# Optimization experiments

Hardware: AMD Instinct MI355X
Metric: run time of the kernel (lower is better)

Reference implementation:

```python
import jax, jax.numpy as jnp
import numpy as np

VOCAB, EMB, HID = 32000, 128, 256
B, T = 512, 512


def setup_inputs() -> dict:
    key = jax.random.key(0)
    ks = jax.random.split(key, 6)
    x = jax.random.randint(ks[0], (B, T), 0, VOCAB, dtype=jnp.int64) if jax.config.jax_enable_x64 else jax.random.randint(ks[0], (B, T), 0, VOCAB, dtype=jnp.int32)
    s_e = 1.0 / np.sqrt(HID)
    emb = jax.random.normal(ks[1], (VOCAB, EMB), dtype=jnp.float32)
    W_ih = jax.random.uniform(ks[2], (3 * HID, EMB), dtype=jnp.float32, minval=-s_e, maxval=s_e)
    W_hh = jax.random.uniform(ks[3], (3 * HID, HID), dtype=jnp.float32, minval=-s_e, maxval=s_e)
    b_ih = jax.random.uniform(ks[4], (3 * HID,), dtype=jnp.float32, minval=-s_e, maxval=s_e)
    b_hh = jax.random.uniform(ks[5], (3 * HID,), dtype=jnp.float32, minval=-s_e, maxval=s_e)
    return {"x": x, "emb": emb, "W_ih": W_ih, "W_hh": W_hh, "b_ih": b_ih, "b_hh": b_hh}


def reference(x, emb, W_ih, W_hh, b_ih, b_hh):
    # in_len = x.shape[0] per original code (loops x[:, t, :] for t in range(x.shape[0]))
    in_len = x.shape[0]
    H = W_hh.shape[1]
    xe = emb[x]                                   # [B, T, E]
    xs = jnp.swapaxes(xe[:, :in_len, :], 0, 1)    # [in_len, B, E]
    # precompute input-side gate projections for all timesteps (one big GEMM)
    gi = jnp.einsum('tbe,ge->tbg', xs, W_ih) + b_ih   # [in_len, B, 3H]

    def step(h, gi_t):
        gh = h @ W_hh.T + b_hh                    # [B, 3H]
        i_r, i_z, i_n = gi_t[:, :H], gi_t[:, H:2*H], gi_t[:, 2*H:]
        h_r, h_z, h_n = gh[:, :H], gh[:, H:2*H], gh[:, 2*H:]
        r = jax.nn.sigmoid(i_r + h_r)
        z = jax.nn.sigmoid(i_z + h_z)
        n = jnp.tanh(i_n + r * h_n)
        h_new = (1.0 - z) * n + z * h
        return h_new, None

    h0 = jnp.zeros((x.shape[0], H), dtype=emb.dtype)  # batch = x.shape[0]
    hT, _ = jax.lax.scan(step, h0, gi)
    return hT
```

## Files before the change

### kernel.cpp

```cpp
#include <hip/hip_runtime.h>


typedef unsigned short ushort_t;
typedef __attribute__((ext_vector_type(8))) short short8;
typedef __attribute__((ext_vector_type(4))) float float4_;
typedef __attribute__((ext_vector_type(4))) unsigned short ushort4_;
typedef __attribute__((ext_vector_type(2))) unsigned int uint2_;

#define VOCAB 32000
#define EMB 128
#define HID 256
#define G3 768
#define BB 512
#define TT 512
#define SLOT 786432
#define BLK_BYTES 24576
#define WFIXED 8781824

__device__ __forceinline__ float b2f(ushort_t u) {
  return __uint_as_float(((unsigned)u) << 16);
}
__device__ __forceinline__ ushort_t f2b(float f) {
  unsigned u = __float_as_uint(f);
  return (ushort_t)((u + 0x7FFFu + ((u >> 16) & 1u)) >> 16);
}
__device__ __forceinline__ short8 ld8(const ushort_t* p) { return *(const short8*)p; }
__device__ __forceinline__ void gld_lds16(const void* g, void* l) {
  __builtin_amdgcn_global_load_lds((const __attribute__((address_space(1))) void*)g,
                                   (__attribute__((address_space(3))) void*)l, 16, 0, 0);
}
__device__ __forceinline__ int gi_byte(int bl, int twog) {
  return ((bl * 1536) + twog) ^ ((bl & 7) << 4);
}

__global__ void cvt_bf16_k(const float* __restrict__ s, ushort_t* __restrict__ d, int n4) {
  int i = blockIdx.x * blockDim.x + threadIdx.x;
  int stride = gridDim.x * blockDim.x;
  for (; i < n4; i += stride) {
    float4_ v = ((const float4_*)s)[i];
    ushort4_ o;
    o.x = f2b(v.x); o.y = f2b(v.y); o.z = f2b(v.z); o.w = f2b(v.w);
    ((ushort4_*)d)[i] = o;
  }
}

__global__ __launch_bounds__(256) void gi_gemm(
    const int* __restrict__ x, const ushort_t* __restrict__ emb16,
    const ushort_t* __restrict__ Wih16, const float* __restrict__ bih,
    const float* __restrict__ bhh, char* __restrict__ gic, int t0, int C) {
  __shared__ float cb[G3];
  __shared__ alignas(16) char img[2][BLK_BYTES];
  const int tid = threadIdx.x;
  for (int i = tid; i < G3; i += 256) cb[i] = bih[i] + (i < 512 ? bhh[i] : 0.f);
  const int lane = tid & 63, w = tid >> 6;
  const int bl = lane & 15, kg = lane >> 4;
  const int blk = blockIdx.x & 31;
  const int tt0 = (blockIdx.x >> 5) * 2;
  const int nj = (C - tt0) < 2 ? 1 : 2;

  short8 bfr[2][4];
#pragma unroll
  for (int j = 0; j < 2; ++j) {
    int tloc = tt0 + (j < nj ? j : 0);
    int tok = x[(blk * 16 + bl) * TT + t0 + tloc];
#pragma unroll
    for (int kt = 0; kt < 4; ++kt)
      bfr[j][kt] = ld8(emb16 + (size_t)tok * EMB + kt * 32 + kg * 8);
  }
  __syncthreads();

#pragma unroll 1
  for (int mi = 0; mi < 12; ++mi) {
    int mt = w * 12 + mi;
    short8 af[4];
#pragma unroll
    for (int kt = 0; kt < 4; ++kt)
      af[kt] = ld8(Wih16 + (mt * 16 + bl) * EMB + kt * 32 + kg * 8);
    float4_ z4 = {0.f, 0.f, 0.f, 0.f};
    float4_ acc[2] = {z4, z4};
#pragma unroll
    for (int kt = 0; kt < 4; ++kt)
#pragma unroll
      for (int j = 0; j < 2; ++j)
        acc[j] = __builtin_amdgcn_mfma_f32_16x16x32_bf16(af[kt], bfr[j][kt], acc[j], 0, 0, 0);
    int byte8 = gi_byte(bl, 32 * mt + 8 * kg);
#pragma unroll
    for (int j = 0; j < 2; ++j) {
      ushort4_ o;
#pragma unroll
      for (int r = 0; r < 4; ++r) o[r] = f2b(acc[j][r] + cb[mt * 16 + kg * 4 + r]);
      *(ushort4_*)(&img[j][byte8]) = o;
    }
  }
  __syncthreads();

#pragma unroll
  for (int j = 0; j < 2; ++j) {
    if (j < nj) {
      char* dst = gic + (size_t)(tt0 + j) * SLOT + (size_t)blk * BLK_BYTES;
#pragma unroll
      for (int c = 0; c < 6; ++c)
        *(float4_*)(dst + c * 4096 + tid * 16) = *(const float4_*)(&img[j][c * 4096 + tid * 16]);
    }
  }
}

__global__ __launch_bounds__(512, 2) void gru_rec(
    const ushort_t* __restrict__ Whh16, const char* __restrict__ gic,
    const float* __restrict__ bhh, float* __restrict__ out, int t0, int C) {
  __shared__ alignas(16) ushort_t h_lds[2][16 * HID];
  __shared__ alignas(16) char gi_ring[4][BLK_BYTES];

  const int tid = threadIdx.x, lane = tid & 63, w = tid >> 6;
  const int bl = lane & 15, kg = lane >> 4;
  const int b0 = blockIdx.x * 16;
  const char* gblk = gic + (size_t)blockIdx.x * BLK_BYTES;

  if (t0 == 0) {
    for (int i = tid; i < 16 * HID; i += 512) h_lds[0][i] = 0;
  } else {
    for (int i = tid; i < 16 * HID; i += 512) {
      int b = i >> 8, k = i & 255;
      *(ushort_t*)((char*)h_lds[0] + (((b << 9) + 2 * k) ^ ((b & 7) << 4))) =
          f2b(out[(size_t)(b0 + b) * HID + k]);
    }
  }

  short8 wf[2][3][8];
#pragma unroll
  for (int i = 0; i < 2; ++i)
#pragma unroll
    for (int q = 0; q < 3; ++q) {
      int g = (w + 8 * i + 16 * q) * 16 + bl;
#pragma unroll
      for (int kt = 0; kt < 8; ++kt)
        wf[i][q][kt] = ld8(Whh16 + (size_t)g * HID + kt * 32 + kg * 8);
    }

  float4_ bhn[2];
  float hreg[2][4];
#pragma unroll
  for (int i = 0; i < 2; ++i) {
    bhn[i] = *(const float4_*)&bhh[512 + (w + 8 * i) * 16 + kg * 4];
    if (t0 == 0) {
#pragma unroll
      for (int r = 0; r < 4; ++r) hreg[i][r] = 0.f;
    } else {
      float4_ v = *(const float4_*)&out[(size_t)(b0 + bl) * HID + (w + 8 * i) * 16 + kg * 4];
#pragma unroll
      for (int r = 0; r < 4; ++r) hreg[i][r] = v[r];
    }
  }

  asm volatile("s_waitcnt vmcnt(0) lgkmcnt(0)" ::: "memory");
  __builtin_amdgcn_s_barrier();
  __builtin_amdgcn_sched_barrier(0);

#pragma unroll
  for (int tau = 0; tau < 3; ++tau) {
    if (tau < C) {
      const char* src = gblk + (size_t)tau * SLOT + (w * 3) * 1024 + lane * 16;
      char* dst = &gi_ring[tau][(w * 3) * 1024];
#pragma unroll
      for (int ii = 0; ii < 3; ++ii) gld_lds16(src + ii * 1024, dst + ii * 1024);
    }
  }

#pragma unroll 1
  for (int t = 0; t < C; ++t) {
    int rem = C - 1 - t;
    if (rem >= 2)
      asm volatile("s_waitcnt vmcnt(6) lgkmcnt(0)" ::: "memory");
    else if (rem == 1)
      asm volatile("s_waitcnt vmcnt(3) lgkmcnt(0)" ::: "memory");
    else
      asm volatile("s_waitcnt vmcnt(0) lgkmcnt(0)" ::: "memory");
    __builtin_amdgcn_s_barrier();
    __builtin_amdgcn_sched_barrier(0);

    const int slot = t & 3, cur = t & 1, nxt = cur ^ 1;
    if (t + 3 < C) {
      const char* src = gblk + (size_t)(t + 3) * SLOT + (w * 3) * 1024 + lane * 16;
      char* dst = &gi_ring[(t + 3) & 3][(w * 3) * 1024];
#pragma unroll
      for (int ii = 0; ii < 3; ++ii) gld_lds16(src + ii * 1024, dst + ii * 1024);
    }

    float4_ acc[2][3];
#pragma unroll
    for (int i = 0; i < 2; ++i) {
#pragma unroll
      for (int q = 0; q < 2; ++q) {
        int byte8 = gi_byte(bl, 32 * (w + 8 * i + 16 * q) + 8 * kg);
        ushort4_ v = *(const ushort4_*)(&gi_ring[slot][byte8]);
#pragma unroll
        for (int r = 0; r < 4; ++r) acc[i][q][r] = b2f(v[r]);
      }
      acc[i][2] = bhn[i];
    }

#pragma unroll
    for (int kt = 0; kt < 8; ++kt) {
      int byteoff = ((bl * 512) + kt * 64 + kg * 16) ^ ((bl & 7) << 4);
      short8 bf = *(const short8*)((const char*)h_lds[cur] + byteoff);
#pragma unroll
      for (int i = 0; i < 2; ++i)
#pragma unroll
        for (int q = 0; q < 3; ++q)
          acc[i][q] = __builtin_amdgcn_mfma_f32_16x16x32_bf16(wf[i][q][kt], bf, acc[i][q], 0, 0, 0);
    }

#pragma unroll
    for (int i = 0; i < 2; ++i) {
      int byte8n = gi_byte(bl, 32 * (32 + w + 8 * i) + 8 * kg);
      ushort4_ gv = *(const ushort4_*)(&gi_ring[slot][byte8n]);
#pragma unroll
      for (int r = 0; r < 4; ++r) {
        float rr = __builtin_amdgcn_rcpf(1.f + __expf(-acc[i][0][r]));
        float zz = __builtin_amdgcn_rcpf(1.f + __expf(-acc[i][1][r]));
        float y = b2f(gv[r]) + rr * acc[i][2][r];
        float nn = 1.f - 2.f * __builtin_amdgcn_rcpf(1.f + __expf(2.f * y));
        hreg[i][r] = (1.f - zz) * nn + zz * hreg[i][r];
      }
      int byte0 = (bl * 512 + ((w + 8 * i) * 16 + kg * 4) * 2) ^ ((bl & 7) << 4);
      uint2_ hv;
      hv.x = (unsigned)f2b(hreg[i][0]) | ((unsigned)f2b(hreg[i][1]) << 16);
      hv.y = (unsigned)f2b(hreg[i][2]) | ((unsigned)f2b(hreg[i][3]) << 16);
      *(uint2_*)((char*)h_lds[nxt] + byte0) = hv;
    }
  }

#pragma unroll
  for (int i = 0; i < 2; ++i) {
    float4_ v = {hreg[i][0], hreg[i][1], hreg[i][2], hreg[i][3]};
    *(float4_*)&out[(size_t)(b0 + bl) * HID + (w + 8 * i) * 16 + kg * 4] = v;
  }
}

extern "C" void kernel_launch(void* const* d_in, const int* in_sizes, int n_in,
                              void* d_out, int out_size, void* d_ws, size_t ws_size,
                              hipStream_t stream) {
  const int* x = (const int*)d_in[0];
  const float* emb = (const float*)d_in[1];
  const float* Wih = (const float*)d_in[2];
  const float* Whh = (const float*)d_in[3];
  const float* bih = (const float*)d_in[4];
  const float* bhh = (const float*)d_in[5];
  float* out = (float*)d_out;

  char* ws = (char*)d_ws;
  ushort_t* emb16 = (ushort_t*)ws;
  ushort_t* Wih16 = (ushort_t*)(ws + 8192000);
  ushort_t* Whh16 = (ushort_t*)(ws + 8388608);
  char* gic = ws + WFIXED;

  size_t avail = ws_size > (size_t)WFIXED ? ws_size - (size_t)WFIXED : 0;
  int C = (int)(avail / (size_t)SLOT);
  if (C > TT) C = TT;
  if (C < 1) C = 1;

  cvt_bf16_k<<<1024, 256, 0, stream>>>(emb, emb16, (VOCAB * EMB) / 4);
  cvt_bf16_k<<<96, 256, 0, stream>>>(Wih, Wih16, (G3 * EMB) / 4);
  cvt_bf16_k<<<192, 256, 0, stream>>>(Whh, Whh16, (G3 * HID) / 4);

  for (int t0 = 0; t0 < TT; t0 += C) {
    int Cc = TT - t0 < C ? TT - t0 : C;
    gi_gemm<<<((Cc + 1) / 2) * 32, 256, 0, stream>>>(x, emb16, Wih16, bih, bhh, gic, t0, Cc);
    gru_rec<<<32, 512, 0, stream>>>(Whh16, gic, bhh, out, t0, Cc);
  }
}
```

Baseline: 1.521 ms.

## Precompute per-vocab input projection table and gather rows in recurrence

Replaces the per-(timestep,batch) input-gate GEMM with a table of W_ih·emb+bias over all 32000 vocab entries. The recurrent kernel then stages tokens in LDS and gathers table rows into its LDS ring with async global-to-LDS loads. This removes the large per-step gi buffer and the chunked launch loop, running the whole sequence in a single recurrence launch. In exchange the table GEMM does 32000 rows of work instead of 512x512, and each step's gathers hit scattered table rows rather than contiguous slots.

```diff
diff --git a/kernel.cpp b/kernel.cpp
--- a/kernel.cpp
+++ b/kernel.cpp
@@ -6,16 +6,15 @@
 typedef __attribute__((ext_vector_type(4))) float float4_;
 typedef __attribute__((ext_vector_type(4))) unsigned short ushort4_;
 typedef __attribute__((ext_vector_type(2))) unsigned int uint2_;
+typedef __attribute__((ext_vector_type(4))) int int4_;
 
 #define VOCAB 32000
 #define EMB 128
 #define HID 256
 #define G3 768
-#define BB 512
 #define TT 512
-#define SLOT 786432
-#define BLK_BYTES 24576
-#define WFIXED 8781824
+#define HB 98304
+#define XB 114688
 
 __device__ __forceinline__ float b2f(ushort_t u) {
   return __uint_as_float(((unsigned)u) << 16);
@@ -29,8 +28,8 @@
   __builtin_amdgcn_global_load_lds((const __attribute__((address_space(1))) void*)g,
                                    (__attribute__((address_space(3))) void*)l, 16, 0, 0);
 }
-__device__ __forceinline__ int gi_byte(int bl, int twog) {
-  return ((bl * 1536) + twog) ^ ((bl & 7) << 4);
+__device__ __forceinline__ int gi_byte(int bl, int c) {
+  return ((bl * 1536) + c) ^ ((bl & 7) << 4);
 }
 
 __global__ void cvt_bf16_k(const float* __restrict__ s, ushort_t* __restrict__ d, int n4) {
@@ -44,29 +43,22 @@
   }
 }
 
-__global__ __launch_bounds__(256) void gi_gemm(
-    const int* __restrict__ x, const ushort_t* __restrict__ emb16,
-    const ushort_t* __restrict__ Wih16, const float* __restrict__ bih,
-    const float* __restrict__ bhh, char* __restrict__ gic, int t0, int C) {
-  __shared__ float cb[G3];
-  __shared__ alignas(16) char img[2][BLK_BYTES];
+__global__ __launch_bounds__(256) void tbl_gemm(
+    const ushort_t* __restrict__ emb16, const ushort_t* __restrict__ Wih16,
+    const float* __restrict__ bih, const float* __restrict__ bhh,
+    char* __restrict__ tb_out) {
+  __shared__ float cbs[G3];
+  __shared__ alignas(16) char img[16 * 1552];
   const int tid = threadIdx.x;
-  for (int i = tid; i < G3; i += 256) cb[i] = bih[i] + (i < 512 ? bhh[i] : 0.f);
+  for (int i = tid; i < G3; i += 256) cbs[i] = bih[i] + (i < 512 ? bhh[i] : 0.f);
   const int lane = tid & 63, w = tid >> 6;
   const int bl = lane & 15, kg = lane >> 4;
-  const int blk = blockIdx.x & 31;
-  const int tt0 = (blockIdx.x >> 5) * 2;
-  const int nj = (C - tt0) < 2 ? 1 : 2;
-
-  short8 bfr[2][4];
-#pragma unroll
-  for (int j = 0; j < 2; ++j) {
-    int tloc = tt0 + (j < nj ? j : 0);
-    int tok = x[(blk * 16 + bl) * TT + t0 + tloc];
-#pragma unroll
-    for (int kt = 0; kt < 4; ++kt)
-      bfr[j][kt] = ld8(emb16 + (size_t)tok * EMB + kt * 32 + kg * 8);
-  }
+  const int v0 = blockIdx.x * 16;
+
+  short8 bfr[4];
+#pragma unroll
+  for (int kt = 0; kt < 4; ++kt)
+    bfr[kt] = ld8(emb16 + (size_t)(v0 + bl) * EMB + kt * 32 + kg * 8);
   __syncthreads();
 
 #pragma unroll 1
@@ -76,55 +68,48 @@
 #pragma unroll
     for (int kt = 0; kt < 4; ++kt)
       af[kt] = ld8(Wih16 + (mt * 16 + bl) * EMB + kt * 32 + kg * 8);
-    float4_ z4 = {0.f, 0.f, 0.f, 0.f};
-    float4_ acc[2] = {z4, z4};
+    float4_ acc = {0.f, 0.f, 0.f, 0.f};
 #pragma unroll
     for (int kt = 0; kt < 4; ++kt)
-#pragma unroll
-      for (int j = 0; j < 2; ++j)
-        acc[j] = __builtin_amdgcn_mfma_f32_16x16x32_bf16(af[kt], bfr[j][kt], acc[j], 0, 0, 0);
-    int byte8 = gi_byte(bl, 32 * mt + 8 * kg);
-#pragma unroll
-    for (int j = 0; j < 2; ++j) {
-      ushort4_ o;
-#pragma unroll
-      for (int r = 0; r < 4; ++r) o[r] = f2b(acc[j][r] + cb[mt * 16 + kg * 4 + r]);
-      *(ushort4_*)(&img[j][byte8]) = o;
-    }
+      acc = __builtin_amdgcn_mfma_f32_16x16x32_bf16(af[kt], bfr[kt], acc, 0, 0, 0);
+    int g0 = mt * 16 + kg * 4;
+    ushort4_ o;
+#pragma unroll
+    for (int r = 0; r < 4; ++r) o[r] = f2b(acc[r] + cbs[g0 + r]);
+    *(ushort4_*)(img + bl * 1552 + mt * 32 + kg * 8) = o;
   }
   __syncthreads();
 
 #pragma unroll
-  for (int j = 0; j < 2; ++j) {
-    if (j < nj) {
-      char* dst = gic + (size_t)(tt0 + j) * SLOT + (size_t)blk * BLK_BYTES;
-#pragma unroll
-      for (int c = 0; c < 6; ++c)
-        *(float4_*)(dst + c * 4096 + tid * 16) = *(const float4_*)(&img[j][c * 4096 + tid * 16]);
-    }
+  for (int c = 0; c < 6; ++c) {
+    int p = c * 4096 + tid * 16;
+    int q = p >> 9;
+    int row = (q * 21846) >> 16;
+    int off = p - row * 1536;
+    float4_ v = *(const float4_*)(img + row * 1552 + off);
+    *(float4_*)(tb_out + (size_t)(v0 + row) * 1536 + off) = v;
   }
 }
 
 __global__ __launch_bounds__(512, 2) void gru_rec(
-    const ushort_t* __restrict__ Whh16, const char* __restrict__ gic,
-    const float* __restrict__ bhh, float* __restrict__ out, int t0, int C) {
-  __shared__ alignas(16) ushort_t h_lds[2][16 * HID];
-  __shared__ alignas(16) char gi_ring[4][BLK_BYTES];
+    const ushort_t* __restrict__ Whh16, const char* __restrict__ tbl,
+    const float* __restrict__ bhh, const int* __restrict__ x,
+    float* __restrict__ out) {
+  __shared__ alignas(16) char smem[147456];
 
   const int tid = threadIdx.x, lane = tid & 63, w = tid >> 6;
   const int bl = lane & 15, kg = lane >> 4;
   const int b0 = blockIdx.x * 16;
-  const char* gblk = gic + (size_t)blockIdx.x * BLK_BYTES;
-
-  if (t0 == 0) {
-    for (int i = tid; i < 16 * HID; i += 512) h_lds[0][i] = 0;
-  } else {
-    for (int i = tid; i < 16 * HID; i += 512) {
-      int b = i >> 8, k = i & 255;
-      *(ushort_t*)((char*)h_lds[0] + (((b << 9) + 2 * k) ^ ((b & 7) << 4))) =
-          f2b(out[(size_t)(b0 + b) * HID + k]);
-    }
-  }
+
+  {
+    const int4_* xs = (const int4_*)(x + (size_t)b0 * TT);
+    int4_* xd = (int4_*)(smem + XB);
+#pragma unroll
+    for (int i = 0; i < 4; ++i) xd[tid + i * 512] = xs[tid + i * 512];
+    int4_ z4 = {0, 0, 0, 0};
+    *(int4_*)(smem + HB + tid * 16) = z4;
+  }
+  __syncthreads();
 
   short8 wf[2][3][8];
 #pragma unroll
@@ -142,33 +127,35 @@
 #pragma unroll
   for (int i = 0; i < 2; ++i) {
     bhn[i] = *(const float4_*)&bhh[512 + (w + 8 * i) * 16 + kg * 4];
-    if (t0 == 0) {
-#pragma unroll
-      for (int r = 0; r < 4; ++r) hreg[i][r] = 0.f;
-    } else {
-      float4_ v = *(const float4_*)&out[(size_t)(b0 + bl) * HID + (w + 8 * i) * 16 + kg * 4];
-#pragma unroll
-      for (int r = 0; r < 4; ++r) hreg[i][r] = v[r];
-    }
-  }
-
-  asm volatile("s_waitcnt vmcnt(0) lgkmcnt(0)" ::: "memory");
-  __builtin_amdgcn_s_barrier();
-  __builtin_amdgcn_sched_barrier(0);
+#pragma unroll
+    for (int r = 0; r < 4; ++r) hreg[i][r] = 0.f;
+  }
+
+  const int s0 = ((2 * w) & 7) << 4, s1 = ((2 * w + 1) & 7) << 4;
+  const unsigned inv0 = (unsigned)((lane * 16) ^ s0);
+  const unsigned inv1 = (lane < 32) ? (unsigned)((1024 + lane * 16) ^ s0)
+                                    : (unsigned)((lane * 16 - 512) ^ s1);
+  const unsigned inv2 = (unsigned)((512 + lane * 16) ^ s1);
+  const int* xtA = (const int*)(smem + XB) + (2 * w) * TT;
+  const int* xtB = (const int*)(smem + XB) + (2 * w + 1) * TT;
+
+  asm volatile("s_waitcnt vmcnt(0)" ::: "memory");
 
 #pragma unroll
   for (int tau = 0; tau < 3; ++tau) {
-    if (tau < C) {
-      const char* src = gblk + (size_t)tau * SLOT + (w * 3) * 1024 + lane * 16;
-      char* dst = &gi_ring[tau][(w * 3) * 1024];
-#pragma unroll
-      for (int ii = 0; ii < 3; ++ii) gld_lds16(src + ii * 1024, dst + ii * 1024);
-    }
+    int tokA = xtA[tau], tokB = xtB[tau];
+    const char* pA = tbl + (unsigned)tokA * 1536u;
+    const char* pB = tbl + (unsigned)tokB * 1536u;
+    const char* pM = (lane < 32) ? pA : pB;
+    char* d0 = smem + tau * 24576 + w * 3072;
+    gld_lds16(pA + inv0, d0);
+    gld_lds16(pM + inv1, d0 + 1024);
+    gld_lds16(pB + inv2, d0 + 2048);
   }
 
 #pragma unroll 1
-  for (int t = 0; t < C; ++t) {
-    int rem = C - 1 - t;
+  for (int t = 0; t < TT; ++t) {
+    int rem = TT - 1 - t;
     if (rem >= 2)
       asm volatile("s_waitcnt vmcnt(6) lgkmcnt(0)" ::: "memory");
     else if (rem == 1)
@@ -179,12 +166,18 @@
     __builtin_amdgcn_sched_barrier(0);
 
     const int slot = t & 3, cur = t & 1, nxt = cur ^ 1;
-    if (t + 3 < C) {
-      const char* src = gblk + (size_t)(t + 3) * SLOT + (w * 3) * 1024 + lane * 16;
-      char* dst = &gi_ring[(t + 3) & 3][(w * 3) * 1024];
-#pragma unroll
-      for (int ii = 0; ii < 3; ++ii) gld_lds16(src + ii * 1024, dst + ii * 1024);
-    }
+    if (t + 3 < TT) {
+      int tokA = xtA[t + 3], tokB = xtB[t + 3];
+      const char* pA = tbl + (unsigned)tokA * 1536u;
+      const char* pB = tbl + (unsigned)tokB * 1536u;
+      const char* pM = (lane < 32) ? pA : pB;
+      char* d0 = smem + ((t + 3) & 3) * 24576 + w * 3072;
+      gld_lds16(pA + inv0, d0);
+      gld_lds16(pM + inv1, d0 + 1024);
+      gld_lds16(pB + inv2, d0 + 2048);
+    }
+
+    const char* gtile = smem + slot * 24576;
 
     float4_ acc[2][3];
 #pragma unroll
@@ -192,7 +185,7 @@
 #pragma unroll
       for (int q = 0; q < 2; ++q) {
         int byte8 = gi_byte(bl, 32 * (w + 8 * i + 16 * q) + 8 * kg);
-        ushort4_ v = *(const ushort4_*)(&gi_ring[slot][byte8]);
+        ushort4_ v = *(const ushort4_*)(gtile + byte8);
 #pragma unroll
         for (int r = 0; r < 4; ++r) acc[i][q][r] = b2f(v[r]);
       }
@@ -202,7 +195,7 @@
 #pragma unroll
     for (int kt = 0; kt < 8; ++kt) {
       int byteoff = ((bl * 512) + kt * 64 + kg * 16) ^ ((bl & 7) << 4);
-      short8 bf = *(const short8*)((const char*)h_lds[cur] + byteoff);
+      short8 bf = *(const short8*)(smem + HB + cur * 8192 + byteoff);
 #pragma unroll
       for (int i = 0; i < 2; ++i)
 #pragma unroll
@@ -213,7 +206,7 @@
 #pragma unroll
     for (int i = 0; i < 2; ++i) {
       int byte8n = gi_byte(bl, 32 * (32 + w + 8 * i) + 8 * kg);
-      ushort4_ gv = *(const ushort4_*)(&gi_ring[slot][byte8n]);
+      ushort4_ gv = *(const ushort4_*)(gtile + byte8n);
 #pragma unroll
       for (int r = 0; r < 4; ++r) {
         float rr = __builtin_amdgcn_rcpf(1.f + __expf(-acc[i][0][r]));
@@ -226,7 +219,7 @@
       uint2_ hv;
       hv.x = (unsigned)f2b(hreg[i][0]) | ((unsigned)f2b(hreg[i][1]) << 16);
       hv.y = (unsigned)f2b(hreg[i][2]) | ((unsigned)f2b(hreg[i][3]) << 16);
-      *(uint2_*)((char*)h_lds[nxt] + byte0) = hv;
+      *(uint2_*)(smem + HB + nxt * 8192 + byte0) = hv;
     }
   }
 
@@ -252,20 +245,11 @@
   ushort_t* emb16 = (ushort_t*)ws;
   ushort_t* Wih16 = (ushort_t*)(ws + 8192000);
   ushort_t* Whh16 = (ushort_t*)(ws + 8388608);
-  char* gic = ws + WFIXED;
-
-  size_t avail = ws_size > (size_t)WFIXED ? ws_size - (size_t)WFIXED : 0;
-  int C = (int)(avail / (size_t)SLOT);
-  if (C > TT) C = TT;
-  if (C < 1) C = 1;
+  char* tbl = ws + 8781824;
 
   cvt_bf16_k<<<1024, 256, 0, stream>>>(emb, emb16, (VOCAB * EMB) / 4);
   cvt_bf16_k<<<96, 256, 0, stream>>>(Wih, Wih16, (G3 * EMB) / 4);
   cvt_bf16_k<<<192, 256, 0, stream>>>(Whh, Whh16, (G3 * HID) / 4);
-
-  for (int t0 = 0; t0 < TT; t0 += C) {
-    int Cc = TT - t0 < C ? TT - t0 : C;
-    gi_gemm<<<((Cc + 1) / 2) * 32, 256, 0, stream>>>(x, emb16, Wih16, bih, bhh, gic, t0, Cc);
-    gru_rec<<<32, 512, 0, stream>>>(Whh16, gic, bhh, out, t0, Cc);
-  }
-}
+  tbl_gemm<<<2000, 256, 0, stream>>>(emb16, Wih16, bih, bhh, tbl);
+  gru_rec<<<32, 512, 0, stream>>>(Whh16, tbl, bhh, x, out);
+}
```

Measured after the change: 1.361 ms. 1.12x faster.

## Precompute per-vocabulary input gate table and gather rows instead of per-token GEMM

Applied to the files above, without the earlier changes.

Computes the input-side gate projection (with biases) once for every vocabulary entry into a bf16 table, then builds the per-timestep gate buffer by gathering table rows by token id. This removes the redundant per-token GEMM, since there are far more tokens than vocabulary entries. In exchange it adds a ~49MB table write and random-row gather reads, and reduces the workspace left for timestep chunks, which may increase the number of chunks.

```diff
diff --git a/kernel.cpp b/kernel.cpp
--- a/kernel.cpp
+++ b/kernel.cpp
@@ -6,16 +6,17 @@
 typedef __attribute__((ext_vector_type(4))) float float4_;
 typedef __attribute__((ext_vector_type(4))) unsigned short ushort4_;
 typedef __attribute__((ext_vector_type(2))) unsigned int uint2_;
+typedef __attribute__((ext_vector_type(4))) int int4_;
 
 #define VOCAB 32000
 #define EMB 128
 #define HID 256
 #define G3 768
-#define BB 512
 #define TT 512
 #define SLOT 786432
 #define BLK_BYTES 24576
-#define WFIXED 8781824
+#define TBL_OFF 8781824
+#define GIC_OFF 57933824
 
 __device__ __forceinline__ float b2f(ushort_t u) {
   return __uint_as_float(((unsigned)u) << 16);
@@ -29,8 +30,8 @@
   __builtin_amdgcn_global_load_lds((const __attribute__((address_space(1))) void*)g,
                                    (__attribute__((address_space(3))) void*)l, 16, 0, 0);
 }
-__device__ __forceinline__ int gi_byte(int bl, int twog) {
-  return ((bl * 1536) + twog) ^ ((bl & 7) << 4);
+__device__ __forceinline__ int gi_byte(int bl, int c) {
+  return ((bl * 1536) + c) ^ ((bl & 7) << 4);
 }
 
 __global__ void cvt_bf16_k(const float* __restrict__ s, ushort_t* __restrict__ d, int n4) {
@@ -44,29 +45,22 @@
   }
 }
 
-__global__ __launch_bounds__(256) void gi_gemm(
-    const int* __restrict__ x, const ushort_t* __restrict__ emb16,
-    const ushort_t* __restrict__ Wih16, const float* __restrict__ bih,
-    const float* __restrict__ bhh, char* __restrict__ gic, int t0, int C) {
-  __shared__ float cb[G3];
-  __shared__ alignas(16) char img[2][BLK_BYTES];
+__global__ __launch_bounds__(256) void tbl_gemm(
+    const ushort_t* __restrict__ emb16, const ushort_t* __restrict__ Wih16,
+    const float* __restrict__ bih, const float* __restrict__ bhh,
+    char* __restrict__ tb_out) {
+  __shared__ float cbs[G3];
+  __shared__ alignas(16) char img[16 * 1552];
   const int tid = threadIdx.x;
-  for (int i = tid; i < G3; i += 256) cb[i] = bih[i] + (i < 512 ? bhh[i] : 0.f);
+  for (int i = tid; i < G3; i += 256) cbs[i] = bih[i] + (i < 512 ? bhh[i] : 0.f);
   const int lane = tid & 63, w = tid >> 6;
   const int bl = lane & 15, kg = lane >> 4;
-  const int blk = blockIdx.x & 31;
-  const int tt0 = (blockIdx.x >> 5) * 2;
-  const int nj = (C - tt0) < 2 ? 1 : 2;
-
-  short8 bfr[2][4];
-#pragma unroll
-  for (int j = 0; j < 2; ++j) {
-    int tloc = tt0 + (j < nj ? j : 0);
-    int tok = x[(blk * 16 + bl) * TT + t0 + tloc];
-#pragma unroll
-    for (int kt = 0; kt < 4; ++kt)
-      bfr[j][kt] = ld8(emb16 + (size_t)tok * EMB + kt * 32 + kg * 8);
-  }
+  const int v0 = blockIdx.x * 16;
+
+  short8 bfr[4];
+#pragma unroll
+  for (int kt = 0; kt < 4; ++kt)
+    bfr[kt] = ld8(emb16 + (size_t)(v0 + bl) * EMB + kt * 32 + kg * 8);
   __syncthreads();
 
 #pragma unroll 1
@@ -76,31 +70,55 @@
 #pragma unroll
     for (int kt = 0; kt < 4; ++kt)
       af[kt] = ld8(Wih16 + (mt * 16 + bl) * EMB + kt * 32 + kg * 8);
-    float4_ z4 = {0.f, 0.f, 0.f, 0.f};
-    float4_ acc[2] = {z4, z4};
+    float4_ acc = {0.f, 0.f, 0.f, 0.f};
 #pragma unroll
     for (int kt = 0; kt < 4; ++kt)
-#pragma unroll
-      for (int j = 0; j < 2; ++j)
-        acc[j] = __builtin_amdgcn_mfma_f32_16x16x32_bf16(af[kt], bfr[j][kt], acc[j], 0, 0, 0);
-    int byte8 = gi_byte(bl, 32 * mt + 8 * kg);
-#pragma unroll
-    for (int j = 0; j < 2; ++j) {
-      ushort4_ o;
-#pragma unroll
-      for (int r = 0; r < 4; ++r) o[r] = f2b(acc[j][r] + cb[mt * 16 + kg * 4 + r]);
-      *(ushort4_*)(&img[j][byte8]) = o;
-    }
+      acc = __builtin_amdgcn_mfma_f32_16x16x32_bf16(af[kt], bfr[kt], acc, 0, 0, 0);
+    int g0 = mt * 16 + kg * 4;
+    ushort4_ o;
+#pragma unroll
+    for (int r = 0; r < 4; ++r) o[r] = f2b(acc[r] + cbs[g0 + r]);
+    *(ushort4_*)(img + bl * 1552 + mt * 32 + kg * 8) = o;
   }
   __syncthreads();
 
 #pragma unroll
-  for (int j = 0; j < 2; ++j) {
-    if (j < nj) {
-      char* dst = gic + (size_t)(tt0 + j) * SLOT + (size_t)blk * BLK_BYTES;
-#pragma unroll
-      for (int c = 0; c < 6; ++c)
-        *(float4_*)(dst + c * 4096 + tid * 16) = *(const float4_*)(&img[j][c * 4096 + tid * 16]);
+  for (int c = 0; c < 6; ++c) {
+    int p = c * 4096 + tid * 16;
+    int q = p >> 9;
+    int row = (q * 21846) >> 16;
+    int off = p - row * 1536;
+    float4_ v = *(const float4_*)(img + row * 1552 + off);
+    *(float4_*)(tb_out + (size_t)(v0 + row) * 1536 + off) = v;
+  }
+}
+
+__global__ __launch_bounds__(256) void gi_mat(
+    const int* __restrict__ x, const char* __restrict__ tbl,
+    char* __restrict__ gic, int tbase, int Cc) {
+  __shared__ int toks[64];
+  const int tg = blockIdx.x >> 5, blk = blockIdx.x & 31;
+  const int tid = threadIdx.x;
+  if (tid < 64) {
+    int j = tid >> 4, row = tid & 15;
+    int tt = 4 * tg + j;
+    toks[tid] = (tt < Cc) ? x[(blk * 16 + row) * TT + tbase + tt] : 0;
+  }
+  __syncthreads();
+  const int row = tid >> 4;
+  const int c0 = (tid & 15) * 16;
+  const int rs = (row & 7) << 4;
+#pragma unroll
+  for (int j = 0; j < 4; ++j) {
+    int tt = 4 * tg + j;
+    if (tt < Cc) {
+      const char* src = tbl + (size_t)toks[j * 16 + row] * 1536u + c0;
+      char* dst = gic + (size_t)tt * SLOT + (size_t)blk * BLK_BYTES;
+#pragma unroll
+      for (int ii = 0; ii < 6; ++ii) {
+        float4_ v = *(const float4_*)(src + ii * 256);
+        *(float4_*)(dst + ((row * 1536 + c0 + ii * 256) ^ rs)) = v;
+      }
     }
   }
 }
@@ -108,8 +126,7 @@
 __global__ __launch_bounds__(512, 2) void gru_rec(
     const ushort_t* __restrict__ Whh16, const char* __restrict__ gic,
     const float* __restrict__ bhh, float* __restrict__ out, int t0, int C) {
-  __shared__ alignas(16) ushort_t h_lds[2][16 * HID];
-  __shared__ alignas(16) char gi_ring[4][BLK_BYTES];
+  __shared__ alignas(16) char smem[114688];
 
   const int tid = threadIdx.x, lane = tid & 63, w = tid >> 6;
   const int bl = lane & 15, kg = lane >> 4;
@@ -117,11 +134,12 @@
   const char* gblk = gic + (size_t)blockIdx.x * BLK_BYTES;
 
   if (t0 == 0) {
-    for (int i = tid; i < 16 * HID; i += 512) h_lds[0][i] = 0;
+    int4_ z4 = {0, 0, 0, 0};
+    *(int4_*)(smem + 98304 + tid * 16) = z4;
   } else {
     for (int i = tid; i < 16 * HID; i += 512) {
       int b = i >> 8, k = i & 255;
-      *(ushort_t*)((char*)h_lds[0] + (((b << 9) + 2 * k) ^ ((b & 7) << 4))) =
+      *(ushort_t*)(smem + 98304 + (((b << 9) + 2 * k) ^ ((b & 7) << 4))) =
           f2b(out[(size_t)(b0 + b) * HID + k]);
     }
   }
@@ -160,7 +178,7 @@
   for (int tau = 0; tau < 3; ++tau) {
     if (tau < C) {
       const char* src = gblk + (size_t)tau * SLOT + (w * 3) * 1024 + lane * 16;
-      char* dst = &gi_ring[tau][(w * 3) * 1024];
+      char* dst = smem + tau * 24576 + (w * 3) * 1024;
 #pragma unroll
       for (int ii = 0; ii < 3; ++ii) gld_lds16(src + ii * 1024, dst + ii * 1024);
     }
@@ -181,10 +199,12 @@
     const int slot = t & 3, cur = t & 1, nxt = cur ^ 1;
     if (t + 3 < C) {
       const char* src = gblk + (size_t)(t + 3) * SLOT + (w * 3) * 1024 + lane * 16;
-      char* dst = &gi_ring[(t + 3) & 3][(w * 3) * 1024];
+      char* dst = smem + ((t + 3) & 3) * 24576 + (w * 3) * 1024;
 #pragma unroll
       for (int ii = 0; ii < 3; ++ii) gld_lds16(src + ii * 1024, dst + ii * 1024);
     }
+
+    const char* gtile = smem + slot * 24576;
 
     float4_ acc[2][3];
 #pragma unroll
@@ -192,7 +212,7 @@
 #pragma unroll
       for (int q = 0; q < 2; ++q) {
         int byte8 = gi_byte(bl, 32 * (w + 8 * i + 16 * q) + 8 * kg);
-        ushort4_ v = *(const ushort4_*)(&gi_ring[slot][byte8]);
+        ushort4_ v = *(const ushort4_*)(gtile + byte8);
 #pragma unroll
         for (int r = 0; r < 4; ++r) acc[i][q][r] = b2f(v[r]);
       }
@@ -202,7 +222,7 @@
 #pragma unroll
     for (int kt = 0; kt < 8; ++kt) {
       int byteoff = ((bl * 512) + kt * 64 + kg * 16) ^ ((bl & 7) << 4);
-      short8 bf = *(const short8*)((const char*)h_lds[cur] + byteoff);
+      short8 bf = *(const short8*)(smem + 98304 + cur * 8192 + byteoff);
 #pragma unroll
       for (int i = 0; i < 2; ++i)
 #pragma unroll
@@ -213,7 +233,7 @@
 #pragma unroll
     for (int i = 0; i < 2; ++i) {
       int byte8n = gi_byte(bl, 32 * (32 + w + 8 * i) + 8 * kg);
-      ushort4_ gv = *(const ushort4_*)(&gi_ring[slot][byte8n]);
+      ushort4_ gv = *(const ushort4_*)(gtile + byte8n);
 #pragma unroll
       for (int r = 0; r < 4; ++r) {
         float rr = __builtin_amdgcn_rcpf(1.f + __expf(-acc[i][0][r]));
@@ -226,7 +246,7 @@
       uint2_ hv;
       hv.x = (unsigned)f2b(hreg[i][0]) | ((unsigned)f2b(hreg[i][1]) << 16);
       hv.y = (unsigned)f2b(hreg[i][2]) | ((unsigned)f2b(hreg[i][3]) << 16);
-      *(uint2_*)((char*)h_lds[nxt] + byte0) = hv;
+      *(uint2_*)(smem + 98304 + nxt * 8192 + byte0) = hv;
     }
   }
 
@@ -252,9 +272,10 @@
   ushort_t* emb16 = (ushort_t*)ws;
   ushort_t* Wih16 = (ushort_t*)(ws + 8192000);
   ushort_t* Whh16 = (ushort_t*)(ws + 8388608);
-  char* gic = ws + WFIXED;
-
-  size_t avail = ws_size > (size_t)WFIXED ? ws_size - (size_t)WFIXED : 0;
+  char* tbl = ws + TBL_OFF;
+  char* gic = ws + GIC_OFF;
+
+  size_t avail = ws_size > (size_t)GIC_OFF ? ws_size - (size_t)GIC_OFF : 0;
   int C = (int)(avail / (size_t)SLOT);
   if (C > TT) C = TT;
   if (C < 1) C = 1;
@@ -262,10 +283,12 @@
   cvt_bf16_k<<<1024, 256, 0, stream>>>(emb, emb16, (VOCAB * EMB) / 4);
   cvt_bf16_k<<<96, 256, 0, stream>>>(Wih, Wih16, (G3 * EMB) / 4);
   cvt_bf16_k<<<192, 256, 0, stream>>>(Whh, Whh16, (G3 * HID) / 4);
+  tbl_gemm<<<2000, 256, 0, stream>>>(emb16, Wih16, bih, bhh, tbl);
 
   for (int t0 = 0; t0 < TT; t0 += C) {
     int Cc = TT - t0 < C ? TT - t0 : C;
-    gi_gemm<<<((Cc + 1) / 2) * 32, 256, 0, stream>>>(x, emb16, Wih16, bih, bhh, gic, t0, Cc);
+    int ntg = (Cc + 3) / 4;
+    gi_mat<<<32 * ntg, 256, 0, stream>>>(x, tbl, gic, t0, Cc);
     gru_rec<<<32, 512, 0, stream>>>(Whh16, gic, bhh, out, t0, Cc);
   }
 }
```

Measured after the change: 1.510 ms. About the same (-0.7%).
